# Kernel optimization log

Measured on AMD Instinct MI355X. Metric: run time of the kernel, lower is better.

## Reference

```python
import jax, jax.numpy as jnp
import numpy as np

NUM_HEADS = 12
LN_EPS = 1e-5


def setup_inputs() -> dict:
    key = jax.random.key(0)
    k1, k2, k3 = jax.random.split(key, 3)
    B, S, E = 8, 1024, 768
    x = jax.random.normal(k1, (B, S, E), dtype=jnp.float32)
    # torch nn.Linear(E, 3E): y = x @ W.T + b. We store the transposed weight [E, 3E].
    w_qkv = jax.random.normal(k2, (E, 3 * E), dtype=jnp.float32) * (1.0 / np.sqrt(E))
    b_qkv = jax.random.normal(k3, (3 * E,), dtype=jnp.float32) * 0.02
    ln_gamma = jnp.ones((E,), dtype=jnp.float32)
    ln_beta = jnp.zeros((E,), dtype=jnp.float32)
    return {"x": x, "w_qkv": w_qkv, "b_qkv": b_qkv, "ln_gamma": ln_gamma, "ln_beta": ln_beta}


def reference(x, w_qkv, b_qkv, ln_gamma, ln_beta):
    B, S, E = x.shape
    H = NUM_HEADS
    D = E // H
    qkv = x @ w_qkv + b_qkv                       # [B, S, 3E]
    qkv = qkv.reshape(B, S, 3, H, D)
    q, k, v = qkv[:, :, 0], qkv[:, :, 1], qkv[:, :, 2]   # each [B, S, H, D]
    scores = jnp.einsum("bshd,bthd->bhst", q, k) / jnp.sqrt(jnp.float32(D))
    attn = jax.nn.softmax(scores, axis=-1)        # [B, H, S, S]
    out = jnp.einsum("bhst,bthd->bshd", attn, v)  # [B, S, H, D]
    # per-head concat in head order == reshape to [B, S, E]
    out = out.reshape(B, S, E)
    y = x + out
    mean = jnp.mean(y, axis=-1, keepdims=True)
    var = jnp.var(y, axis=-1, keepdims=True)
    y = (y - mean) * jax.lax.rsqrt(var + LN_EPS)
    return y * ln_gamma + ln_beta
```

## Files before the change

### kernel.cpp

```cpp
#include <hip/hip_runtime.h>

typedef __attribute__((ext_vector_type(8))) short short8;
typedef __attribute__((ext_vector_type(4))) float f32x4;

#define DEVI __device__ __forceinline__

DEVI unsigned fbits(float f) { return __builtin_bit_cast(unsigned, f); }
DEVI unsigned short f2bf(float f) {
    unsigned u = __builtin_bit_cast(unsigned, f);
    u += 0x7fffu + ((u >> 16) & 1u);
    return (unsigned short)(u >> 16);
}
DEVI unsigned pktrunc(float a, float b) {
    return __builtin_amdgcn_perm(fbits(b), fbits(a), 0x07060302u);
}

__global__ void ktrans(const float* __restrict__ w,
                       unsigned short* __restrict__ wt) {
    __shared__ float t[32][33];
    const int tx = threadIdx.x, ty = threadIdx.y;
    const int n0 = blockIdx.x * 32, k0 = blockIdx.y * 32;
#pragma unroll
    for (int i = 0; i < 4; i++)
        t[ty + i * 8][tx] = w[(k0 + ty + i * 8) * 2304 + n0 + tx];
    __syncthreads();
#pragma unroll
    for (int i = 0; i < 4; i++)
        wt[(n0 + ty + i * 8) * 768 + k0 + tx] = f2bf(t[tx][ty + i * 8]);
}

#define AST 40
__global__ __launch_bounds__(256) void kgemm(
        const float* __restrict__ A,
        const unsigned short* __restrict__ Bt,
        const float* __restrict__ bias,
        unsigned short* __restrict__ q,
        unsigned short* __restrict__ k_,
        unsigned short* __restrict__ vt) {
    __shared__ __align__(16) unsigned short As[128 * AST];
    __shared__ __align__(16) unsigned short Bs[128 * AST];
    const int tid = threadIdx.x;
    const int w = tid >> 6, lane = tid & 63;
    const int wm = w >> 1, wn = w & 1;
    const int m0 = blockIdx.y * 128, n0 = blockIdx.x * 128;

    f32x4 acc[4][4] = {};

    const int frow = lane & 15;
    const int fkof = (lane >> 4) * 8;

    for (int kk = 0; kk < 768; kk += 32) {
        __syncthreads();
#pragma unroll
        for (int j = 0; j < 2; j++) {
            const int e = (tid + j * 256) * 8;
            const int row = e >> 5, col = e & 31;
            const float4 a0 = *(const float4*)&A[(m0 + row) * 768 + kk + col];
            const float4 a1 = *(const float4*)&A[(m0 + row) * 768 + kk + col + 4];
            uint4 pk;
            pk.x = pktrunc(a0.x, a0.y);
            pk.y = pktrunc(a0.z, a0.w);
            pk.z = pktrunc(a1.x, a1.y);
            pk.w = pktrunc(a1.z, a1.w);
            *(uint4*)&As[row * AST + col] = pk;
            *(short8*)&Bs[row * AST + col] = *(const short8*)&Bt[(n0 + row) * 768 + kk + col];
        }
        __syncthreads();
        short8 af[4], bf[4];
#pragma unroll
        for (int mi = 0; mi < 4; mi++)
            af[mi] = *(const short8*)&As[(wm * 64 + mi * 16 + frow) * AST + fkof];
#pragma unroll
        for (int ni = 0; ni < 4; ni++)
            bf[ni] = *(const short8*)&Bs[(wn * 64 + ni * 16 + frow) * AST + fkof];
#pragma unroll
        for (int mi = 0; mi < 4; mi++)
#pragma unroll
            for (int ni = 0; ni < 4; ni++)
                acc[mi][ni] = __builtin_amdgcn_mfma_f32_16x16x32_bf16(
                    af[mi], bf[ni], acc[mi][ni], 0, 0, 0);
    }

    const int col0 = n0 + wn * 64;
    const int row0 = m0 + wm * 64;
#pragma unroll
    for (int mi = 0; mi < 4; mi++) {
#pragma unroll
        for (int ni = 0; ni < 4; ni++) {
            const int n_ = col0 + ni * 16 + (lane & 15);
            const float bv = bias[n_];
            const int which = n_ / 768;
            const int r7 = n_ % 768;
            const int h = r7 >> 6, d = r7 & 63;
#pragma unroll
            for (int r = 0; r < 4; r++) {
                const int m_ = row0 + mi * 16 + (lane >> 4) * 4 + r;
                const int bb = m_ >> 10, s = m_ & 1023;
                const int bh = bb * 12 + h;
                const unsigned short o = f2bf(acc[mi][ni][r] + bv);
                if (which == 0)      q[(bh * 1024 + s) * 64 + d] = o;
                else if (which == 1) k_[(bh * 1024 + s) * 64 + d] = o;
                else                 vt[(bh * 64 + d) * 1024 + s] = o;
            }
        }
    }
}

#define SCL 0.18033688011112042f
#define KST 72

__global__ __launch_bounds__(256) void kattn(
        const unsigned short* __restrict__ q,
        const unsigned short* __restrict__ k_,
        const unsigned short* __restrict__ vt,
        float* __restrict__ out) {
    __shared__ __align__(16) unsigned short Ks[64 * KST];
    __shared__ __align__(16) unsigned short Vs[64 * KST];
    __shared__ __align__(16) unsigned short Ps[4][32 * KST];
    const int tid = threadIdx.x;
    const int w = tid >> 6, lane = tid & 63;
    const int bh = blockIdx.x;
    const int qt = blockIdx.y;
    const int bb = bh / 12, h = bh % 12;
    const unsigned short* qb = q + bh * 1024 * 64;
    const unsigned short* kb = k_ + bh * 1024 * 64;
    const unsigned short* vb = vt + bh * 64 * 1024;

    const int frow = lane & 15;
    const int grp = lane >> 4;
    const int m0 = qt * 128 + w * 32;

    short8 qf[2][2];
#pragma unroll
    for (int mi = 0; mi < 2; mi++)
#pragma unroll
        for (int ks = 0; ks < 2; ks++)
            qf[mi][ks] = *(const short8*)&qb[(m0 + mi * 16 + frow) * 64 + ks * 32 + grp * 8];

    f32x4 oacc[2][4] = {};
    float rmax[2] = {-INFINITY, -INFINITY}, rsum[2] = {0.f, 0.f};

    for (int t0 = 0; t0 < 1024; t0 += 64) {
        __syncthreads();
#pragma unroll
        for (int j = 0; j < 2; j++) {
            const int e = (tid + j * 256) * 8;
            const int row = e >> 6, col = e & 63;
            *(short8*)&Ks[row * KST + col] = *(const short8*)&kb[(t0 + row) * 64 + col];
            *(short8*)&Vs[row * KST + col] = *(const short8*)&vb[row * 1024 + t0 + col];
        }
        __syncthreads();

        f32x4 sacc[4][2] = {};
#pragma unroll
        for (int ks = 0; ks < 2; ks++) {
            short8 kf[4];
#pragma unroll
            for (int ni = 0; ni < 4; ni++)
                kf[ni] = *(const short8*)&Ks[(ni * 16 + frow) * KST + ks * 32 + grp * 8];
#pragma unroll
            for (int ni = 0; ni < 4; ni++)
#pragma unroll
                for (int mi = 0; mi < 2; mi++)
                    sacc[ni][mi] = __builtin_amdgcn_mfma_f32_16x16x32_bf16(
                        kf[ni], qf[mi][ks], sacc[ni][mi], 0, 0, 0);
        }

#pragma unroll
        for (int mi = 0; mi < 2; mi++) {
            float mt = -INFINITY;
#pragma unroll
            for (int ni = 0; ni < 4; ni++)
#pragma unroll
                for (int r = 0; r < 4; r++) mt = fmaxf(mt, sacc[ni][mi][r]);
            mt = fmaxf(mt, __shfl_xor(mt, 16, 64));
            mt = fmaxf(mt, __shfl_xor(mt, 32, 64));
            const float mnew = fmaxf(rmax[mi], mt);
            const float alpha = exp2f((rmax[mi] - mnew) * SCL);
            rmax[mi] = mnew;
            const float mb = mnew * SCL;
            float ps = 0.f;
#pragma unroll
            for (int ni = 0; ni < 4; ni++)
#pragma unroll
                for (int r = 0; r < 4; r++) {
                    const float p = exp2f(sacc[ni][mi][r] * SCL - mb);
                    sacc[ni][mi][r] = p;
                    ps += p;
                }
            ps += __shfl_xor(ps, 16, 64);
            ps += __shfl_xor(ps, 32, 64);
            rsum[mi] = rsum[mi] * alpha + ps;
#pragma unroll
            for (int di = 0; di < 4; di++) oacc[mi][di] *= alpha;
#pragma unroll
            for (int ni = 0; ni < 4; ni++) {
                uint2 pk;
                pk.x = pktrunc(sacc[ni][mi][0], sacc[ni][mi][1]);
                pk.y = pktrunc(sacc[ni][mi][2], sacc[ni][mi][3]);
                *(uint2*)&Ps[w][(mi * 16 + frow) * KST + ni * 16 + grp * 4] = pk;
            }
        }

#pragma unroll
        for (int ks = 0; ks < 2; ks++) {
            short8 vf[4], pf[2];
#pragma unroll
            for (int di = 0; di < 4; di++)
                vf[di] = *(const short8*)&Vs[(di * 16 + frow) * KST + ks * 32 + grp * 8];
#pragma unroll
            for (int mi = 0; mi < 2; mi++)
                pf[mi] = *(const short8*)&Ps[w][(mi * 16 + frow) * KST + ks * 32 + grp * 8];
#pragma unroll
            for (int mi = 0; mi < 2; mi++)
#pragma unroll
                for (int di = 0; di < 4; di++)
                    oacc[mi][di] = __builtin_amdgcn_mfma_f32_16x16x32_bf16(
                        vf[di], pf[mi], oacc[mi][di], 0, 0, 0);
        }
    }

#pragma unroll
    for (int mi = 0; mi < 2; mi++) {
        const float inv = 1.0f / rsum[mi];
        const int s = m0 + mi * 16 + frow;
#pragma unroll
        for (int di = 0; di < 4; di++) {
            f32x4 o = oacc[mi][di] * inv;
            const int d0 = di * 16 + grp * 4;
            *(f32x4*)&out[(bb * 1024 + s) * 768 + h * 64 + d0] = o;
        }
    }
}

__global__ __launch_bounds__(256) void kln(
        const float* __restrict__ x,
        const float* __restrict__ gamma,
        const float* __restrict__ beta,
        float* __restrict__ out) {
    __shared__ float red[8];
    const int row = blockIdx.x;
    const int tid = threadIdx.x;
    const float* xr = x + row * 768;
    float* orow = out + row * 768;
    float y[3], sum = 0.f, sumsq = 0.f;
#pragma unroll
    for (int i = 0; i < 3; i++) {
        const int e = tid + i * 256;
        const float v = xr[e] + orow[e];
        y[i] = v; sum += v; sumsq += v * v;
    }
#pragma unroll
    for (int o = 1; o < 64; o <<= 1) {
        sum += __shfl_xor(sum, o, 64);
        sumsq += __shfl_xor(sumsq, o, 64);
    }
    const int w = tid >> 6, lane = tid & 63;
    if (lane == 0) { red[w] = sum; red[4 + w] = sumsq; }
    __syncthreads();
    sum = red[0] + red[1] + red[2] + red[3];
    sumsq = red[4] + red[5] + red[6] + red[7];
    const float mean = sum * (1.0f / 768.0f);
    const float var = sumsq * (1.0f / 768.0f) - mean * mean;
    const float rs = rsqrtf(var + 1e-5f);
#pragma unroll
    for (int i = 0; i < 3; i++) {
        const int e = tid + i * 256;
        orow[e] = (y[i] - mean) * rs * gamma[e] + beta[e];
    }
}

extern "C" void kernel_launch(void* const* d_in, const int* in_sizes, int n_in,
                              void* d_out, int out_size, void* d_ws, size_t ws_size,
                              hipStream_t stream) {
    (void)in_sizes; (void)n_in; (void)out_size; (void)ws_size;
    const float* x     = (const float*)d_in[0];
    const float* wqkv  = (const float*)d_in[1];
    const float* bqkv  = (const float*)d_in[2];
    const float* gamma = (const float*)d_in[3];
    const float* beta  = (const float*)d_in[4];
    float* out = (float*)d_out;
    unsigned short* ws = (unsigned short*)d_ws;

    unsigned short* wt = ws;
    unsigned short* q  = wt + 2304 * 768;
    unsigned short* k  = q + 96 * 1024 * 64;
    unsigned short* vt = k + 96 * 1024 * 64;

    ktrans<<<dim3(72, 24), dim3(32, 8), 0, stream>>>(wqkv, wt);
    kgemm<<<dim3(18, 64), 256, 0, stream>>>(x, wt, bqkv, q, k, vt);
    kattn<<<dim3(96, 8), 256, 0, stream>>>(q, k, vt, out);
    kln<<<8192, 256, 0, stream>>>(x, gamma, beta, out);
}
```

Baseline: 245.8 us.

## Load GEMM and attention tiles with direct global-to-LDS async loads in fragment layout

```diff
diff --git a/kernel.cpp b/kernel.cpp
--- a/kernel.cpp
+++ b/kernel.cpp
@@ -14,6 +14,22 @@
 DEVI unsigned pktrunc(float a, float b) {
     return __builtin_amdgcn_perm(fbits(b), fbits(a), 0x07060302u);
 }
+DEVI void async16(const unsigned short* g, unsigned short* l) {
+    __builtin_amdgcn_global_load_lds(
+        (const __attribute__((address_space(1))) void*)g,
+        (__attribute__((address_space(3))) void*)l,
+        16, 0, 0);
+}
+
+__global__ __launch_bounds__(256) void kcvt(const float* __restrict__ x,
+                                            unsigned short* __restrict__ xb) {
+    const int i = (blockIdx.x * 256 + threadIdx.x) * 4;
+    const float4 v = *(const float4*)&x[i];
+    uint2 pk;
+    pk.x = (unsigned)f2bf(v.x) | ((unsigned)f2bf(v.y) << 16);
+    pk.y = (unsigned)f2bf(v.z) | ((unsigned)f2bf(v.w) << 16);
+    *(uint2*)&xb[i] = pk;
+}
 
 __global__ void ktrans(const float* __restrict__ w,
                        unsigned short* __restrict__ wt) {
@@ -29,50 +45,39 @@
         wt[(n0 + ty + i * 8) * 768 + k0 + tx] = f2bf(t[tx][ty + i * 8]);
 }
 
-#define AST 40
 __global__ __launch_bounds__(256) void kgemm(
-        const float* __restrict__ A,
-        const unsigned short* __restrict__ Bt,
+        const unsigned short* __restrict__ xb,
+        const unsigned short* __restrict__ wt,
         const float* __restrict__ bias,
         unsigned short* __restrict__ q,
         unsigned short* __restrict__ k_,
         unsigned short* __restrict__ vt) {
-    __shared__ __align__(16) unsigned short As[128 * AST];
-    __shared__ __align__(16) unsigned short Bs[128 * AST];
+    __shared__ __align__(16) unsigned short As[8 * 512];
+    __shared__ __align__(16) unsigned short Bs[8 * 512];
     const int tid = threadIdx.x;
     const int w = tid >> 6, lane = tid & 63;
     const int wm = w >> 1, wn = w & 1;
     const int m0 = blockIdx.y * 128, n0 = blockIdx.x * 128;
+    const int gr = lane & 15, gc = (lane >> 4) * 8;
 
     f32x4 acc[4][4] = {};
-
-    const int frow = lane & 15;
-    const int fkof = (lane >> 4) * 8;
 
     for (int kk = 0; kk < 768; kk += 32) {
         __syncthreads();
 #pragma unroll
         for (int j = 0; j < 2; j++) {
-            const int e = (tid + j * 256) * 8;
-            const int row = e >> 5, col = e & 31;
-            const float4 a0 = *(const float4*)&A[(m0 + row) * 768 + kk + col];
-            const float4 a1 = *(const float4*)&A[(m0 + row) * 768 + kk + col + 4];
-            uint4 pk;
-            pk.x = pktrunc(a0.x, a0.y);
-            pk.y = pktrunc(a0.z, a0.w);
-            pk.z = pktrunc(a1.x, a1.y);
-            pk.w = pktrunc(a1.z, a1.w);
-            *(uint4*)&As[row * AST + col] = pk;
-            *(short8*)&Bs[row * AST + col] = *(const short8*)&Bt[(n0 + row) * 768 + kk + col];
+            const int t = w + j * 4;
+            async16(&xb[(m0 + t * 16 + gr) * 768 + kk + gc], &As[t * 512]);
+            async16(&wt[(n0 + t * 16 + gr) * 768 + kk + gc], &Bs[t * 512]);
         }
         __syncthreads();
         short8 af[4], bf[4];
 #pragma unroll
         for (int mi = 0; mi < 4; mi++)
-            af[mi] = *(const short8*)&As[(wm * 64 + mi * 16 + frow) * AST + fkof];
+            af[mi] = *(const short8*)&As[(wm * 4 + mi) * 512 + lane * 8];
 #pragma unroll
         for (int ni = 0; ni < 4; ni++)
-            bf[ni] = *(const short8*)&Bs[(wn * 64 + ni * 16 + frow) * AST + fkof];
+            bf[ni] = *(const short8*)&Bs[(wn * 4 + ni) * 512 + lane * 8];
 #pragma unroll
         for (int mi = 0; mi < 4; mi++)
 #pragma unroll
@@ -107,16 +112,15 @@
 }
 
 #define SCL 0.18033688011112042f
-#define KST 72
 
 __global__ __launch_bounds__(256) void kattn(
         const unsigned short* __restrict__ q,
         const unsigned short* __restrict__ k_,
         const unsigned short* __restrict__ vt,
         float* __restrict__ out) {
-    __shared__ __align__(16) unsigned short Ks[64 * KST];
-    __shared__ __align__(16) unsigned short Vs[64 * KST];
-    __shared__ __align__(16) unsigned short Ps[4][32 * KST];
+    __shared__ __align__(16) unsigned short Ks[8 * 512];
+    __shared__ __align__(16) unsigned short Vs[8 * 512];
+    __shared__ __align__(16) unsigned short Ps[4][4 * 512];
     const int tid = threadIdx.x;
     const int w = tid >> 6, lane = tid & 63;
     const int bh = blockIdx.x;
@@ -144,10 +148,9 @@
         __syncthreads();
 #pragma unroll
         for (int j = 0; j < 2; j++) {
-            const int e = (tid + j * 256) * 8;
-            const int row = e >> 6, col = e & 63;
-            *(short8*)&Ks[row * KST + col] = *(const short8*)&kb[(t0 + row) * 64 + col];
-            *(short8*)&Vs[row * KST + col] = *(const short8*)&vb[row * 1024 + t0 + col];
+            const int t = w * 2 + j, ti = t >> 1, ks = t & 1;
+            async16(&kb[(t0 + ti * 16 + frow) * 64 + ks * 32 + grp * 8], &Ks[t * 512]);
+            async16(&vb[(ti * 16 + frow) * 1024 + t0 + ks * 32 + grp * 8], &Vs[t * 512]);
         }
         __syncthreads();
 
@@ -157,7 +160,7 @@
             short8 kf[4];
 #pragma unroll
             for (int ni = 0; ni < 4; ni++)
-                kf[ni] = *(const short8*)&Ks[(ni * 16 + frow) * KST + ks * 32 + grp * 8];
+                kf[ni] = *(const short8*)&Ks[(ni * 2 + ks) * 512 + lane * 8];
 #pragma unroll
             for (int ni = 0; ni < 4; ni++)
 #pragma unroll
@@ -198,7 +201,8 @@
                 uint2 pk;
                 pk.x = pktrunc(sacc[ni][mi][0], sacc[ni][mi][1]);
                 pk.y = pktrunc(sacc[ni][mi][2], sacc[ni][mi][3]);
-                *(uint2*)&Ps[w][(mi * 16 + frow) * KST + ni * 16 + grp * 4] = pk;
+                const int dlane = frow + (((ni << 1) + (grp >> 1)) & 3) * 16;
+                *(uint2*)&Ps[w][(mi * 2 + (ni >> 1)) * 512 + dlane * 8 + (grp & 1) * 4] = pk;
             }
         }
 
@@ -207,10 +211,10 @@
             short8 vf[4], pf[2];
 #pragma unroll
             for (int di = 0; di < 4; di++)
-                vf[di] = *(const short8*)&Vs[(di * 16 + frow) * KST + ks * 32 + grp * 8];
+                vf[di] = *(const short8*)&Vs[(di * 2 + ks) * 512 + lane * 8];
 #pragma unroll
             for (int mi = 0; mi < 2; mi++)
-                pf[mi] = *(const short8*)&Ps[w][(mi * 16 + frow) * KST + ks * 32 + grp * 8];
+                pf[mi] = *(const short8*)&Ps[w][(mi * 2 + ks) * 512 + lane * 8];
 #pragma unroll
             for (int mi = 0; mi < 2; mi++)
 #pragma unroll
@@ -283,12 +287,14 @@
     unsigned short* ws = (unsigned short*)d_ws;
 
     unsigned short* wt = ws;
-    unsigned short* q  = wt + 2304 * 768;
+    unsigned short* xb = wt + 2304 * 768;
+    unsigned short* q  = xb + 8192 * 768;
     unsigned short* k  = q + 96 * 1024 * 64;
     unsigned short* vt = k + 96 * 1024 * 64;
 
+    kcvt<<<6144, 256, 0, stream>>>(x, xb);
     ktrans<<<dim3(72, 24), dim3(32, 8), 0, stream>>>(wqkv, wt);
-    kgemm<<<dim3(18, 64), 256, 0, stream>>>(x, wt, bqkv, q, k, vt);
+    kgemm<<<dim3(18, 64), 256, 0, stream>>>(xb, wt, bqkv, q, k, vt);
     kattn<<<dim3(96, 8), 256, 0, stream>>>(q, k, vt, out);
     kln<<<8192, 256, 0, stream>>>(x, gamma, beta, out);
 }
```

New measurement: 269.1 us. 9.5% more time.
